# Kernel optimization log

Hardware: AMD Instinct MI355X
Metric: run time of the kernel (lower is better)

## Reference

```python
import jax, jax.numpy as jnp
import numpy as np

S, B, D = 4096, 4, 1024
APERTURE = 256
SCALE = 1.0 / np.sqrt(D)
EPS = 1e-6
NEG_INF = -jnp.inf


def _xavier(key, shape, gain=np.sqrt(2.0)):
    fan_in, fan_out = shape[1], shape[0]
    a = gain * np.sqrt(6.0 / (fan_in + fan_out))
    return jax.random.uniform(key, shape, jnp.float32, -a, a)


def setup_inputs() -> dict:
    key = jax.random.key(0)
    ks = jax.random.split(key, 8)
    return {
        "x": jax.random.normal(ks[0], (S, B, D), jnp.float32),
        "Wk": _xavier(ks[1], (D, D)),
        "Wq": _xavier(ks[2], (D, D)),
        "Wv": _xavier(ks[3], (D, D)),
        "Wp": _xavier(ks[4], (D, D)),
        "W1": _xavier(ks[5], (D, D)),
        "b1": jnp.full((D,), 0.1, jnp.float32),
        "W2": _xavier(ks[6], (1, D)),
        "b2": jnp.full((1,), 0.1, jnp.float32),
        "gamma": jnp.ones((D,), jnp.float32),
        "beta": jnp.zeros((D,), jnp.float32),
    }


def _layer_norm(y, gamma, beta):
    m = jnp.mean(y, axis=-1, keepdims=True)
    v = jnp.mean((y - m) ** 2, axis=-1, keepdims=True)
    return (y - m) * jax.lax.rsqrt(v + EPS) * gamma + beta


def reference(x, Wk, Wq, Wv, Wp, W1, b1, W2, b2, gamma, beta):
    # x: (S, B, D) -> (B, S, D)
    xb = jnp.transpose(x, (1, 0, 2))
    K = jnp.einsum('bsd,ed->bse', xb, Wk)
    Q = jnp.einsum('bsd,ed->bse', xb, Wq)
    V = jnp.einsum('bsd,ed->bse', xb, Wv)
    e = jnp.einsum('bqd,bkd->bqk', Q, K) * SCALE  # (B, S, S)
    # ignore_self: -inf on diagonal
    eye = jnp.eye(S, dtype=bool)
    e = jnp.where(eye[None, :, :], NEG_INF, e)
    # aperture mask: torch masks where tril(e,ap)*triu(e,-ap) == 0
    scope = jnp.tril(e, APERTURE) * jnp.triu(e, -APERTURE)
    e = jnp.where(scope == 0, NEG_INF, e)
    alpha = jax.nn.softmax(e, axis=2)  # dropout is identity at eval
    c = jnp.einsum('bqk,bkd->bqd', alpha, V)
    c = jnp.einsum('bqd,ed->bqe', c, Wp)
    y = c + xb
    y = _layer_norm(y, gamma, beta)
    y = jax.nn.relu(jnp.einsum('bsd,ed->bse', y, W1) + b1)
    y = _layer_norm(y, gamma, beta)
    y = jax.nn.sigmoid(jnp.einsum('bsd,ed->bse', y, W2) + b2)  # (B, S, 1)
    return jnp.transpose(y, (1, 0, 2))  # (S, B, 1)
```

## Files before the change

### kernel.cpp

```cpp
#include <hip/hip_runtime.h>
#include <stdint.h>
#include <math.h>

#define S_LEN 4096
#define BATCH 4
#define DIM   1024
#define AP    256
#define NBLK  32
#define BANDC 640
#define SCALE 0.03125f

typedef __attribute__((ext_vector_type(4))) float f32x4;
typedef __attribute__((ext_vector_type(8))) short bf16x8;

__device__ __forceinline__ ushort f2bf(float f) {
  union { float f; uint32_t u; } v; v.f = f;
  uint32_t r = v.u + 0x7FFFu + ((v.u >> 16) & 1u);
  return (ushort)(r >> 16);
}
__device__ __forceinline__ float bf2f(ushort u) {
  union { uint32_t u; float f; } v; v.u = ((uint32_t)u) << 16; return v.f;
}

__device__ __forceinline__ void gload16(const void* g, void* l) {
  __builtin_amdgcn_global_load_lds((const __attribute__((address_space(1))) void*)g,
                                   (__attribute__((address_space(3))) void*)l,
                                   16, 0, 0);
}

__device__ __forceinline__ float block_sum(float v, float* red) {
  #pragma unroll
  for (int o = 32; o > 0; o >>= 1) v += __shfl_xor(v, o, 64);
  const int w = threadIdx.x >> 6;
  if ((threadIdx.x & 63) == 0) red[w] = v;
  __syncthreads();
  v = red[0] + red[1] + red[2] + red[3];
  __syncthreads();
  return v;
}

__device__ __forceinline__ float block_max(float v, float* red) {
  #pragma unroll
  for (int o = 32; o > 0; o >>= 1) v = fmaxf(v, __shfl_xor(v, o, 64));
  const int w = threadIdx.x >> 6;
  if ((threadIdx.x & 63) == 0) red[w] = v;
  __syncthreads();
  v = fmaxf(fmaxf(red[0], red[1]), fmaxf(red[2], red[3]));
  __syncthreads();
  return v;
}

#define STAGE2(dstbase, g0, g1, kcol) \
  gload16((g0) + (kcol), lds + (dstbase) + stOff); \
  gload16((g1) + (kcol), lds + (dstbase) + 4096 + stOff);

#define MFMA16(arow, av, bv) \
  __builtin_amdgcn_s_setprio(1); \
  _Pragma("unroll") for (int m = 0; m < 4; ++m) \
  _Pragma("unroll") for (int n = 0; n < 4; ++n) \
    acc[(arow) + m][n] = __builtin_amdgcn_mfma_f32_16x16x32_bf16(av[m], bv[n], acc[(arow) + m][n], 0, 0, 0); \
  __builtin_amdgcn_s_setprio(0);

#define PHASE_CUT() \
  __builtin_amdgcn_sched_barrier(0); \
  asm volatile("s_barrier" ::: "memory");

__device__ __forceinline__ void gemm256_core(
    const ushort* __restrict__ Ablk, int lda,
    const ushort* __restrict__ Bblk, int ldb,
    int K, ushort* __restrict__ lds,
    f32x4 acc[8][4])
{
  const int tid  = threadIdx.x;
  const int lane = tid & 63;
  const int wave = tid >> 6;
  const int wr = wave >> 2;
  const int wn = wave & 3;

  const int srow = tid >> 2;
  const int gseg = (tid & 3) ^ ((tid >> 3) & 3);
  const ushort* gA0 = Ablk + (size_t)srow * lda + gseg * 8;
  const ushort* gA1 = Ablk + (size_t)(srow + 128) * lda + gseg * 8;
  const ushort* gB0 = Bblk + (size_t)srow * ldb + gseg * 8;
  const ushort* gB1 = Bblk + (size_t)(srow + 128) * ldb + gseg * 8;
  const int stOff = wave * 512;

  const int l15 = lane & 15;
  const int seg = (lane >> 4) ^ ((lane >> 1) & 3);
  const int raBase = (wr * 128 + l15) * 32 + seg * 8;
  const int rbBase = (wn * 64  + l15) * 32 + seg * 8;

  const int NT = K >> 6;

  STAGE2(0,     gA0, gA1, 0)
  STAGE2(16384, gB0, gB1, 0)
  STAGE2(8192,  gA0, gA1, 32)
  STAGE2(24576, gB0, gB1, 32)
  asm volatile("s_waitcnt vmcnt(4)" ::: "memory");
  asm volatile("s_barrier" ::: "memory");

  bf16x8 aE[4], aO[4], bE[4], bO[4];
  #pragma unroll
  for (int m = 0; m < 4; ++m) aE[m] = *(const bf16x8*)(lds + raBase + m * 512);
  #pragma unroll
  for (int n = 0; n < 4; ++n) bE[n] = *(const bf16x8*)(lds + 16384 + rbBase + n * 512);

  for (int t = 0; t < NT; ++t) {
    const int rb = (t & 1) * 32768;
    const int sb = rb ^ 32768;
    const int k1 = (t + 1) << 6;
    const bool more = (t + 1 < NT);

    #pragma unroll
    for (int m = 0; m < 4; ++m) aO[m] = *(const bf16x8*)(lds + rb + raBase + (m + 4) * 512);
    if (more) {
      STAGE2(sb,         gA0, gA1, k1)
      STAGE2(sb + 16384, gB0, gB1, k1)
    }
    MFMA16(0, aE, bE)
    if (more) asm volatile("s_waitcnt vmcnt(4)" ::: "memory");
    else      asm volatile("s_waitcnt vmcnt(0)" ::: "memory");
    PHASE_CUT()

    #pragma unroll
    for (int m = 0; m < 4; ++m) aE[m] = *(const bf16x8*)(lds + rb + 8192 + raBase + m * 512);
    #pragma unroll
    for (int n = 0; n < 4; ++n) bO[n] = *(const bf16x8*)(lds + rb + 24576 + rbBase + n * 512);
    if (more) {
      STAGE2(sb + 8192,  gA0, gA1, k1 + 32)
      STAGE2(sb + 24576, gB0, gB1, k1 + 32)
    }
    MFMA16(4, aO, bE)
    PHASE_CUT()

    #pragma unroll
    for (int m = 0; m < 4; ++m) aO[m] = *(const bf16x8*)(lds + rb + 8192 + raBase + (m + 4) * 512);
    MFMA16(0, aE, bO)
    if (more) asm volatile("s_waitcnt vmcnt(4)" ::: "memory");
    PHASE_CUT()

    if (more) {
      #pragma unroll
      for (int m = 0; m < 4; ++m) aE[m] = *(const bf16x8*)(lds + sb + raBase + m * 512);
      #pragma unroll
      for (int n = 0; n < 4; ++n) bE[n] = *(const bf16x8*)(lds + sb + 16384 + rbBase + n * 512);
    }
    MFMA16(4, aO, bO)
    PHASE_CUT()
  }
}

#define ACC256_ZERO(acc) \
  _Pragma("unroll") for (int m_ = 0; m_ < 8; m_++) \
  _Pragma("unroll") for (int n_ = 0; n_ < 4; n_++) \
  _Pragma("unroll") for (int r_ = 0; r_ < 4; r_++) acc[m_][n_][r_] = 0.0f;

__device__ __forceinline__ void epi256_store_bf16(
    f32x4 acc[8][4], ushort* __restrict__ lds,
    ushort* __restrict__ dst, int rowbase, int colb)
{
  __syncthreads();
  const int lane_ = threadIdx.x & 63;
  const int wave_ = threadIdx.x >> 6;
  const int wrb_ = (wave_ >> 2) * 128;
  const int wnb_ = (wave_ & 3) * 64;
  const int rb_ = (lane_ >> 4) << 2;
  const int cb_ = lane_ & 15;
  #pragma unroll
  for (int m = 0; m < 8; m++)
    #pragma unroll
    for (int n = 0; n < 4; n++)
      #pragma unroll
      for (int r = 0; r < 4; r++) {
        const int rl = wrb_ + m * 16 + rb_ + r;
        const int cl = wnb_ + n * 16 + cb_;
        const int cs = cl ^ (((rl >> 2) & 3) << 4);
        lds[rl * 256 + cs] = f2bf(acc[m][n][r]);
      }
  __syncthreads();
  #pragma unroll
  for (int it = 0; it < 16; ++it) {
    const int chunk = it * 512 + threadIdx.x;
    const int rl = chunk >> 5;
    const int c16 = chunk & 31;
    const int csw = (c16 * 16) ^ (((rl >> 2) & 3) << 5);
    bf16x8 v = *(const bf16x8*)((const char*)lds + rl * 512 + csw);
    *(bf16x8*)(dst + (size_t)(rowbase + rl) * DIM + colb + c16 * 8) = v;
  }
}

__device__ __forceinline__ void epi256_store_relu_bf16(
    f32x4 acc[8][4], ushort* __restrict__ lds,
    ushort* __restrict__ dst, int rowbase, int colb,
    const float* __restrict__ bias)
{
  __syncthreads();
  const int lane_ = threadIdx.x & 63;
  const int wave_ = threadIdx.x >> 6;
  const int wrb_ = (wave_ >> 2) * 128;
  const int wnb_ = (wave_ & 3) * 64;
  const int rb_ = (lane_ >> 4) << 2;
  const int cb_ = lane_ & 15;
  #pragma unroll
  for (int m = 0; m < 8; m++)
    #pragma unroll
    for (int n = 0; n < 4; n++) {
      const int cl = wnb_ + n * 16 + cb_;
      const float bv = bias[colb + cl];
      #pragma unroll
      for (int r = 0; r < 4; r++) {
        const int rl = wrb_ + m * 16 + rb_ + r;
        const int cs = cl ^ (((rl >> 2) & 3) << 4);
        lds[rl * 256 + cs] = f2bf(fmaxf(acc[m][n][r] + bv, 0.0f));
      }
    }
  __syncthreads();
  #pragma unroll
  for (int it = 0; it < 16; ++it) {
    const int chunk = it * 512 + threadIdx.x;
    const int rl = chunk >> 5;
    const int c16 = chunk & 31;
    const int csw = (c16 * 16) ^ (((rl >> 2) & 3) << 5);
    bf16x8 v = *(const bf16x8*)((const char*)lds + rl * 512 + csw);
    *(bf16x8*)(dst + (size_t)(rowbase + rl) * DIM + colb + c16 * 8) = v;
  }
}

#define EPI256_BEGIN(acc) { \
  const int lane_ = threadIdx.x & 63; \
  const int wave_ = threadIdx.x >> 6; \
  const int wrb_ = (wave_ >> 2) * 128; \
  const int wnb_ = (wave_ & 3) * 64; \
  const int rb_ = (lane_ >> 4) << 2; \
  const int cb_ = lane_ & 15; \
  _Pragma("unroll") for (int m_ = 0; m_ < 8; m_++) \
  _Pragma("unroll") for (int n_ = 0; n_ < 4; n_++) \
  _Pragma("unroll") for (int r_ = 0; r_ < 4; r_++) { \
    const int rloc = wrb_ + m_ * 16 + rb_ + r_; \
    const int cloc = wnb_ + n_ * 16 + cb_; \
    const float aval = acc[m_][n_][r_];
#define EPI256_END() } }

__device__ __forceinline__ void gemm_core(
    const ushort* __restrict__ Ablk, int lda,
    const ushort* __restrict__ Bblk, int ldb,
    int k_begin, int k_end,
    ushort* __restrict__ lds,
    f32x4 acc[4][4])
{
  const int tid  = threadIdx.x;
  const int lane = tid & 63;
  const int wr = ((tid >> 7) & 1) * 64;
  const int wc = ((tid >> 6) & 1) * 64;
  const int lr = lane & 15;
  const int seg = (lane >> 4) ^ ((lane >> 1) & 3);

  const int srow = tid >> 2;
  const int gseg = (tid & 3) ^ ((tid >> 3) & 3);
  const ushort* gA0 = Ablk + (size_t)srow * lda + gseg * 8;
  const ushort* gA1 = Ablk + (size_t)(srow + 64) * lda + gseg * 8;
  const ushort* gB0 = Bblk + (size_t)srow * ldb + gseg * 8;
  const ushort* gB1 = Bblk + (size_t)(srow + 64) * ldb + gseg * 8;
  const int stA = (tid >> 6) * 512;

  const int NT = (k_end - k_begin) >> 5;

  gload16(gA0 + k_begin, lds + stA);
  gload16(gA1 + k_begin, lds + 2048 + stA);
  gload16(gB0 + k_begin, lds + 4096 + stA);
  gload16(gB1 + k_begin, lds + 6144 + stA);

  for (int t = 0; t < NT; ++t) {
    if (t + 1 < NT) {
      ushort* buf = lds + ((t + 1) & 1) * 8192;
      const int k0 = k_begin + (t + 1) * 32;
      gload16(gA0 + k0, buf + stA);
      gload16(gA1 + k0, buf + 2048 + stA);
      gload16(gB0 + k0, buf + 4096 + stA);
      gload16(gB1 + k0, buf + 6144 + stA);
      asm volatile("s_waitcnt vmcnt(4)" ::: "memory");
    } else {
      asm volatile("s_waitcnt vmcnt(0)" ::: "memory");
    }
    __builtin_amdgcn_s_barrier();

    const ushort* buf = lds + (t & 1) * 8192;
    bf16x8 af[4], bfv[4];
    #pragma unroll
    for (int m = 0; m < 4; m++)
      af[m] = *(const bf16x8*)(buf + (wr + m * 16 + lr) * 32 + seg * 8);
    #pragma unroll
    for (int n = 0; n < 4; n++)
      bfv[n] = *(const bf16x8*)(buf + 4096 + (wc + n * 16 + lr) * 32 + seg * 8);

    __builtin_amdgcn_s_setprio(1);
    #pragma unroll
    for (int m = 0; m < 4; m++)
      #pragma unroll
      for (int n = 0; n < 4; n++)
        acc[m][n] = __builtin_amdgcn_mfma_f32_16x16x32_bf16(af[m], bfv[n], acc[m][n], 0, 0, 0);
    __builtin_amdgcn_s_setprio(0);
    asm volatile("s_waitcnt lgkmcnt(0)" ::: "memory");
  }
}

#define ACC_ZERO(acc) \
  _Pragma("unroll") for (int m_ = 0; m_ < 4; m_++) \
  _Pragma("unroll") for (int n_ = 0; n_ < 4; n_++) \
  _Pragma("unroll") for (int r_ = 0; r_ < 4; r_++) acc[m_][n_][r_] = 0.0f;

#define EPI_BEGIN(acc) { \
  const int lane_ = threadIdx.x & 63; \
  const int wr_ = ((threadIdx.x >> 7) & 1) * 64; \
  const int wc_ = ((threadIdx.x >> 6) & 1) * 64; \
  const int rb_ = (lane_ >> 4) << 2; \
  const int cb_ = lane_ & 15; \
  _Pragma("unroll") for (int m_ = 0; m_ < 4; m_++) \
  _Pragma("unroll") for (int n_ = 0; n_ < 4; n_++) \
  _Pragma("unroll") for (int r_ = 0; r_ < 4; r_++) { \
    const int rloc = wr_ + m_ * 16 + rb_ + r_; \
    const int cloc = wc_ + n_ * 16 + cb_; \
    const float aval = acc[m_][n_][r_];
#define EPI_END() } }

__global__ __launch_bounds__(256) void prep_x(const float* __restrict__ x, ushort* __restrict__ xb) {
  size_t idx = ((size_t)blockIdx.x * 256 + threadIdx.x) * 4;
  int d = (int)(idx & 1023);
  int s = (int)((idx >> 10) & 4095);
  int b = (int)(idx >> 22);
  float4 v = *(const float4*)(x + ((size_t)s * BATCH + b) * DIM + d);
  ushort4 o;
  o.x = f2bf(v.x); o.y = f2bf(v.y); o.z = f2bf(v.z); o.w = f2bf(v.w);
  *(ushort4*)(xb + idx) = o;
}

__global__ __launch_bounds__(256) void f2bf_all(
    const float* __restrict__ Wk, const float* __restrict__ Wq, const float* __restrict__ Wv,
    const float* __restrict__ Wp, const float* __restrict__ W1,
    ushort* __restrict__ wqkv, ushort* __restrict__ wpb, ushort* __restrict__ w1b)
{
  const int g = blockIdx.x;
  const int which = g >> 10;
  const int idx = ((g & 1023) * 256 + threadIdx.x) * 4;
  const float* src = (which == 0) ? Wk : (which == 1) ? Wq : (which == 2) ? Wv
                   : (which == 3) ? Wp : W1;
  ushort* dst = (which == 0) ? wqkv : (which == 1) ? wqkv + 1048576
              : (which == 2) ? wqkv + 2097152 : (which == 3) ? wpb : w1b;
  float4 v = *(const float4*)(src + idx);
  ushort4 o;
  o.x = f2bf(v.x); o.y = f2bf(v.y); o.z = f2bf(v.z); o.w = f2bf(v.w);
  *(ushort4*)(dst + idx) = o;
}

__global__ __launch_bounds__(512, 2) void qkv_gemm256(
    const ushort* __restrict__ xb, const ushort* __restrict__ wqkv,
    ushort* __restrict__ Kp, ushort* __restrict__ Qp, ushort* __restrict__ Vp)
{
  __shared__ ushort lds[65536];
  const int nid = (blockIdx.x & 7) * 96 + (blockIdx.x >> 3);
  const int by = nid / 12;
  const int bx = nid % 12;
  f32x4 acc[8][4];
  ACC256_ZERO(acc)
  gemm256_core(xb + (size_t)by * 256 * DIM, DIM,
               wqkv + (size_t)bx * 256 * DIM, DIM, DIM, lds, acc);
  ushort* dst = (bx < 4) ? Kp : (bx < 8) ? Qp : Vp;
  epi256_store_bf16(acc, lds, dst, by * 256, (bx & 3) * 256);
}

__global__ __launch_bounds__(512, 2) void wp_gemm256(
    const ushort* __restrict__ cbuf, const ushort* __restrict__ wpb,
    const float* __restrict__ x, float* __restrict__ y0)
{
  __shared__ ushort lds[65536];
  const int nid = (blockIdx.x & 7) * 32 + (blockIdx.x >> 3);
  const int by = nid >> 2;
  const int bx = nid & 3;
  f32x4 acc[8][4];
  ACC256_ZERO(acc)
  gemm256_core(cbuf + (size_t)by * 256 * DIM, DIM,
               wpb + (size_t)bx * 256 * DIM, DIM, DIM, lds, acc);
  EPI256_BEGIN(acc)
    int row = by * 256 + rloc;
    int col = bx * 256 + cloc;
    int b = row >> 12, s = row & 4095;
    y0[(size_t)row * DIM + col] = aval + x[((size_t)s * BATCH + b) * DIM + col];
  EPI256_END()
}

__global__ __launch_bounds__(512, 2) void ffn1_gemm256(
    const ushort* __restrict__ y1, const ushort* __restrict__ w1b,
    const float* __restrict__ b1, ushort* __restrict__ h0)
{
  __shared__ ushort lds[65536];
  const int nid = (blockIdx.x & 7) * 32 + (blockIdx.x >> 3);
  const int by = nid >> 2;
  const int bx = nid & 3;
  f32x4 acc[8][4];
  ACC256_ZERO(acc)
  gemm256_core(y1 + (size_t)by * 256 * DIM, DIM,
               w1b + (size_t)bx * 256 * DIM, DIM, DIM, lds, acc);
  epi256_store_relu_bf16(acc, lds, h0, by * 256, bx * 256, b1);
}

__global__ __launch_bounds__(256) void transpose_v(const ushort* __restrict__ V, ushort* __restrict__ VT) {
  __shared__ ushort tile[64][66];
  const int s0 = blockIdx.x * 64, d0 = blockIdx.y * 64, b = blockIdx.z;
  const ushort* Vb = V + (size_t)b * S_LEN * DIM;
  ushort* VTb = VT + (size_t)b * DIM * S_LEN;
  #pragma unroll
  for (int it = 0; it < 16; it++) {
    int flat = it * 256 + threadIdx.x;
    int r = flat >> 6, c = flat & 63;
    tile[r][c] = Vb[(size_t)(s0 + r) * DIM + d0 + c];
  }
  __syncthreads();
  #pragma unroll
  for (int it = 0; it < 16; it++) {
    int flat = it * 256 + threadIdx.x;
    int r = flat >> 6, c = flat & 63;
    VTb[(size_t)(d0 + r) * S_LEN + s0 + c] = tile[c][r];
  }
}

__global__ __launch_bounds__(256) void scores_gemm(
    const ushort* __restrict__ Qp, const ushort* __restrict__ Kp,
    float* __restrict__ eband)
{
  const int nid = (blockIdx.x & 7) * 80 + (blockIdx.x >> 3);
  const int b   = nid / 160;
  const int rem = nid % 160;
  const int i   = rem / 5;
  const int jj  = rem % 5;
  const int j   = i - 2 + jj;
  if (j < 0 || j >= NBLK) return;
  __shared__ ushort lds[16384];
  f32x4 acc[4][4];
  ACC_ZERO(acc)
  gemm_core(Qp + ((size_t)b * S_LEN + i * 128) * DIM, DIM,
            Kp + ((size_t)b * S_LEN + j * 128) * DIM, DIM, 0, DIM, lds, acc);
  EPI_BEGIN(acc)
    int q = i * 128 + rloc;
    int k = j * 128 + cloc;
    float v = aval * SCALE;
    int dqk = q - k;
    if (dqk == 0 || dqk > AP || dqk < -AP) v = -INFINITY;
    eband[((size_t)b * S_LEN + q) * BANDC + jj * 128 + cloc] = v;
  EPI_END()
}

__global__ __launch_bounds__(256) void softmax_band(const float* __restrict__ eband,
                                                    ushort* __restrict__ aband)
{
  __shared__ float red[4];
  const int qg = blockIdx.x;
  const int s  = qg & 4095;
  const int i  = s >> 7;
  const float* row = eband + (size_t)qg * BANDC;
  ushort* arow = aband + (size_t)qg * BANDC;

  float vals[3];
  bool  valid[3];
  float mx = -INFINITY;
  #pragma unroll
  for (int t = 0; t < 3; t++) {
    int idx = threadIdx.x + t * 256;
    int jj = idx >> 7;
    int j = i - 2 + jj;
    bool ok = (idx < BANDC) && (j >= 0) && (j < NBLK);
    valid[t] = ok;
    float v = ok ? row[idx] : -INFINITY;
    vals[t] = v;
    mx = fmaxf(mx, v);
  }
  float bmax = block_max(mx, red);
  float ss = 0.0f;
  #pragma unroll
  for (int t = 0; t < 3; t++) {
    float e = valid[t] ? __expf(vals[t] - bmax) : 0.0f;
    vals[t] = e;
    ss += e;
  }
  float inv = 1.0f / block_sum(ss, red);
  #pragma unroll
  for (int t = 0; t < 3; t++) {
    int idx = threadIdx.x + t * 256;
    if (idx < BANDC) arow[idx] = f2bf(vals[t] * inv);
  }
}

__global__ __launch_bounds__(256) void av_gemm(
    const ushort* __restrict__ aband, const ushort* __restrict__ VT,
    ushort* __restrict__ cbuf)
{
  const int nid = (blockIdx.x & 7) * 128 + (blockIdx.x >> 3);
  const int by = nid >> 3;
  const int b = by >> 5, i = by & 31;
  const int bx = nid & 7;
  const int jj_lo = (i < 2) ? (2 - i) : 0;
  const int jj_hi = (i > 29) ? (34 - i) : 5;
  __shared__ ushort lds[16384];
  f32x4 acc[4][4];
  ACC_ZERO(acc)
  const ushort* Ablk = aband + ((size_t)b * S_LEN + i * 128) * BANDC;
  const ushort* Bblk = VT + (size_t)b * DIM * S_LEN + (size_t)bx * 128 * S_LEN + (i - 2) * 128;
  gemm_core(Ablk, BANDC, Bblk, S_LEN, jj_lo * 128, jj_hi * 128, lds, acc);

  __syncthreads();
  {
    const int lane_ = threadIdx.x & 63;
    const int wr_ = ((threadIdx.x >> 7) & 1) * 64;
    const int wc_ = ((threadIdx.x >> 6) & 1) * 64;
    const int rb_ = (lane_ >> 4) << 2;
    const int cb_ = lane_ & 15;
    #pragma unroll
    for (int m = 0; m < 4; m++)
      #pragma unroll
      for (int n = 0; n < 4; n++)
        #pragma unroll
        for (int r = 0; r < 4; r++) {
          const int rl = wr_ + m * 16 + rb_ + r;
          const int cl = wc_ + n * 16 + cb_;
          const int cs = cl ^ (((rl >> 2) & 3) << 4);
          lds[rl * 128 + cs] = f2bf(acc[m][n][r]);
        }
  }
  __syncthreads();
  ushort* dst = cbuf + ((size_t)b * S_LEN + i * 128) * DIM + bx * 128;
  #pragma unroll
  for (int it = 0; it < 8; ++it) {
    const int chunk = it * 256 + threadIdx.x;
    const int rl = chunk >> 4;
    const int c16 = chunk & 15;
    const int csw = (c16 * 16) ^ (((rl >> 2) & 3) << 5);
    bf16x8 v = *(const bf16x8*)((const char*)lds + rl * 256 + csw);
    *(bf16x8*)(dst + (size_t)rl * DIM + c16 * 8) = v;
  }
}

__global__ __launch_bounds__(256) void ln_kernel(const float* __restrict__ y0, ushort* __restrict__ y1,
                                                 const float* __restrict__ gamma, const float* __restrict__ beta)
{
  __shared__ float red[4];
  const size_t q = blockIdx.x;
  const int d0 = threadIdx.x * 4;
  float4 v = *(const float4*)(y0 + q * DIM + d0);
  float mean = block_sum(v.x + v.y + v.z + v.w, red) * (1.0f / DIM);
  float q2 = (v.x - mean) * (v.x - mean) + (v.y - mean) * (v.y - mean)
           + (v.z - mean) * (v.z - mean) + (v.w - mean) * (v.w - mean);
  float var = block_sum(q2, red) * (1.0f / DIM);
  float rstd = rsqrtf(var + 1e-6f);
  float4 g = *(const float4*)(gamma + d0);
  float4 bb = *(const float4*)(beta + d0);
  ushort4 o;
  o.x = f2bf((v.x - mean) * rstd * g.x + bb.x);
  o.y = f2bf((v.y - mean) * rstd * g.y + bb.y);
  o.z = f2bf((v.z - mean) * rstd * g.z + bb.z);
  o.w = f2bf((v.w - mean) * rstd * g.w + bb.w);
  *(ushort4*)(y1 + q * DIM + d0) = o;
}

__global__ __launch_bounds__(256) void head_kernel(const ushort* __restrict__ h0,
    const float* __restrict__ gamma, const float* __restrict__ beta,
    const float* __restrict__ W2, const float* __restrict__ b2,
    float* __restrict__ out)
{
  __shared__ float red[4];
  const int qg = blockIdx.x;
  const int b = qg >> 12, s = qg & 4095;
  const int d0 = threadIdx.x * 4;
  ushort4 u = *(const ushort4*)(h0 + (size_t)qg * DIM + d0);
  float v0 = bf2f(u.x), v1 = bf2f(u.y), v2 = bf2f(u.z), v3 = bf2f(u.w);
  float mean = block_sum(v0 + v1 + v2 + v3, red) * (1.0f / DIM);
  float q2 = (v0 - mean) * (v0 - mean) + (v1 - mean) * (v1 - mean)
           + (v2 - mean) * (v2 - mean) + (v3 - mean) * (v3 - mean);
  float var = block_sum(q2, red) * (1.0f / DIM);
  float rstd = rsqrtf(var + 1e-6f);
  float4 g = *(const float4*)(gamma + d0);
  float4 bb = *(const float4*)(beta + d0);
  float4 w2 = *(const float4*)(W2 + d0);
  float part = ((v0 - mean) * rstd * g.x + bb.x) * w2.x
             + ((v1 - mean) * rstd * g.y + bb.y) * w2.y
             + ((v2 - mean) * rstd * g.z + bb.z) * w2.z
             + ((v3 - mean) * rstd * g.w + bb.w) * w2.w;
  float logit = block_sum(part, red) + b2[0];
  if (threadIdx.x == 0) out[(size_t)s * BATCH + b] = 1.0f / (1.0f + expf(-logit));
}

extern "C" void kernel_launch(void* const* d_in, const int* in_sizes, int n_in,
                              void* d_out, int out_size, void* d_ws, size_t ws_size,
                              hipStream_t stream) {
  const float* x     = (const float*)d_in[0];
  const float* Wk    = (const float*)d_in[1];
  const float* Wq    = (const float*)d_in[2];
  const float* Wv    = (const float*)d_in[3];
  const float* Wp    = (const float*)d_in[4];
  const float* W1    = (const float*)d_in[5];
  const float* b1    = (const float*)d_in[6];
  const float* W2    = (const float*)d_in[7];
  const float* b2    = (const float*)d_in[8];
  const float* gamma = (const float*)d_in[9];
  const float* beta  = (const float*)d_in[10];
  float* out = (float*)d_out;

  char* w = (char*)d_ws;
  ushort* xb   = (ushort*)(w + 0);
  ushort* wqkv = (ushort*)(w + 33554432);
  ushort* wpb  = (ushort*)(w + 39845888);
  ushort* w1b  = (ushort*)(w + 41943040);
  ushort* Qp   = (ushort*)(w + 44040192);
  ushort* Kp   = (ushort*)(w + 77594624);
  ushort* Vp   = (ushort*)(w + 111149056);
  ushort* VT   = (ushort*)(w + 144703488);
  float*  big  = (float*)(w + 178257920);
  ushort* aband = Qp;
  ushort* cbuf  = Kp;
  ushort* y1    = Vp;
  ushort* h0    = xb;
  float* eband = big;
  float* y0    = big;

  prep_x<<<16384, 256, 0, stream>>>(x, xb);
  f2bf_all<<<5120, 256, 0, stream>>>(Wk, Wq, Wv, Wp, W1, wqkv, wpb, w1b);

  qkv_gemm256<<<768, 512, 0, stream>>>(xb, wqkv, Kp, Qp, Vp);
  transpose_v<<<dim3(64, 16, 4), 256, 0, stream>>>(Vp, VT);
  scores_gemm<<<640, 256, 0, stream>>>(Qp, Kp, eband);
  softmax_band<<<16384, 256, 0, stream>>>(eband, aband);
  av_gemm<<<1024, 256, 0, stream>>>(aband, VT, cbuf);
  wp_gemm256<<<256, 512, 0, stream>>>(cbuf, wpb, x, y0);
  ln_kernel<<<16384, 256, 0, stream>>>(y0, y1, gamma, beta);
  ffn1_gemm256<<<256, 512, 0, stream>>>(y1, w1b, b1, h0);
  head_kernel<<<16384, 256, 0, stream>>>(h0, gamma, beta, W2, b2, out);
}
```

Before: 373.5 us.

## Move banded attention to 256-tile GEMMs, fp16 scores, wave-per-row norms

Replaces the 128-tile scores and AV GEMMs with the 256x256 gemm256 core over a 768-wide band (3 key blocks), and stores the masked scores as fp16 instead of fp32. Softmax, layernorm and the head kernel now use one wave per row with shuffle-only reductions instead of block reductions with LDS and barriers. This targets score-buffer traffic, sync overhead and per-tile GEMM efficiency. The trade-off is more wasted band work (768 vs 640 columns, fully masked edge tiles) and fp16 range and precision on the scores.

```diff
diff --git a/kernel.cpp b/kernel.cpp
--- a/kernel.cpp
+++ b/kernel.cpp
@@ -6,8 +6,7 @@
 #define BATCH 4
 #define DIM   1024
 #define AP    256
-#define NBLK  32
-#define BANDC 640
+#define BANDC 768
 #define SCALE 0.03125f
 
 typedef __attribute__((ext_vector_type(4))) float f32x4;
@@ -21,6 +20,12 @@
 __device__ __forceinline__ float bf2f(ushort u) {
   union { uint32_t u; float f; } v; v.u = ((uint32_t)u) << 16; return v.f;
 }
+__device__ __forceinline__ ushort f2h(float f) {
+  union { _Float16 h; ushort u; } v; v.h = (_Float16)f; return v.u;
+}
+__device__ __forceinline__ float h2f(ushort u) {
+  union { ushort u; _Float16 h; } v; v.u = u; return (float)v.h;
+}
 
 __device__ __forceinline__ void gload16(const void* g, void* l) {
   __builtin_amdgcn_global_load_lds((const __attribute__((address_space(1))) void*)g,
@@ -28,25 +33,14 @@
                                    16, 0, 0);
 }
 
-__device__ __forceinline__ float block_sum(float v, float* red) {
+__device__ __forceinline__ float wave_sum(float v) {
   #pragma unroll
   for (int o = 32; o > 0; o >>= 1) v += __shfl_xor(v, o, 64);
-  const int w = threadIdx.x >> 6;
-  if ((threadIdx.x & 63) == 0) red[w] = v;
-  __syncthreads();
-  v = red[0] + red[1] + red[2] + red[3];
-  __syncthreads();
   return v;
 }
-
-__device__ __forceinline__ float block_max(float v, float* red) {
+__device__ __forceinline__ float wave_max(float v) {
   #pragma unroll
   for (int o = 32; o > 0; o >>= 1) v = fmaxf(v, __shfl_xor(v, o, 64));
-  const int w = threadIdx.x >> 6;
-  if ((threadIdx.x & 63) == 0) red[w] = v;
-  __syncthreads();
-  v = fmaxf(fmaxf(red[0], red[1]), fmaxf(red[2], red[3]));
-  __syncthreads();
   return v;
 }
 
@@ -241,88 +235,6 @@
     const float aval = acc[m_][n_][r_];
 #define EPI256_END() } }
 
-__device__ __forceinline__ void gemm_core(
-    const ushort* __restrict__ Ablk, int lda,
-    const ushort* __restrict__ Bblk, int ldb,
-    int k_begin, int k_end,
-    ushort* __restrict__ lds,
-    f32x4 acc[4][4])
-{
-  const int tid  = threadIdx.x;
-  const int lane = tid & 63;
-  const int wr = ((tid >> 7) & 1) * 64;
-  const int wc = ((tid >> 6) & 1) * 64;
-  const int lr = lane & 15;
-  const int seg = (lane >> 4) ^ ((lane >> 1) & 3);
-
-  const int srow = tid >> 2;
-  const int gseg = (tid & 3) ^ ((tid >> 3) & 3);
-  const ushort* gA0 = Ablk + (size_t)srow * lda + gseg * 8;
-  const ushort* gA1 = Ablk + (size_t)(srow + 64) * lda + gseg * 8;
-  const ushort* gB0 = Bblk + (size_t)srow * ldb + gseg * 8;
-  const ushort* gB1 = Bblk + (size_t)(srow + 64) * ldb + gseg * 8;
-  const int stA = (tid >> 6) * 512;
-
-  const int NT = (k_end - k_begin) >> 5;
-
-  gload16(gA0 + k_begin, lds + stA);
-  gload16(gA1 + k_begin, lds + 2048 + stA);
-  gload16(gB0 + k_begin, lds + 4096 + stA);
-  gload16(gB1 + k_begin, lds + 6144 + stA);
-
-  for (int t = 0; t < NT; ++t) {
-    if (t + 1 < NT) {
-      ushort* buf = lds + ((t + 1) & 1) * 8192;
-      const int k0 = k_begin + (t + 1) * 32;
-      gload16(gA0 + k0, buf + stA);
-      gload16(gA1 + k0, buf + 2048 + stA);
-      gload16(gB0 + k0, buf + 4096 + stA);
-      gload16(gB1 + k0, buf + 6144 + stA);
-      asm volatile("s_waitcnt vmcnt(4)" ::: "memory");
-    } else {
-      asm volatile("s_waitcnt vmcnt(0)" ::: "memory");
-    }
-    __builtin_amdgcn_s_barrier();
-
-    const ushort* buf = lds + (t & 1) * 8192;
-    bf16x8 af[4], bfv[4];
-    #pragma unroll
-    for (int m = 0; m < 4; m++)
-      af[m] = *(const bf16x8*)(buf + (wr + m * 16 + lr) * 32 + seg * 8);
-    #pragma unroll
-    for (int n = 0; n < 4; n++)
-      bfv[n] = *(const bf16x8*)(buf + 4096 + (wc + n * 16 + lr) * 32 + seg * 8);
-
-    __builtin_amdgcn_s_setprio(1);
-    #pragma unroll
-    for (int m = 0; m < 4; m++)
-      #pragma unroll
-      for (int n = 0; n < 4; n++)
-        acc[m][n] = __builtin_amdgcn_mfma_f32_16x16x32_bf16(af[m], bfv[n], acc[m][n], 0, 0, 0);
-    __builtin_amdgcn_s_setprio(0);
-    asm volatile("s_waitcnt lgkmcnt(0)" ::: "memory");
-  }
-}
-
-#define ACC_ZERO(acc) \
-  _Pragma("unroll") for (int m_ = 0; m_ < 4; m_++) \
-  _Pragma("unroll") for (int n_ = 0; n_ < 4; n_++) \
-  _Pragma("unroll") for (int r_ = 0; r_ < 4; r_++) acc[m_][n_][r_] = 0.0f;
-
-#define EPI_BEGIN(acc) { \
-  const int lane_ = threadIdx.x & 63; \
-  const int wr_ = ((threadIdx.x >> 7) & 1) * 64; \
-  const int wc_ = ((threadIdx.x >> 6) & 1) * 64; \
-  const int rb_ = (lane_ >> 4) << 2; \
-  const int cb_ = lane_ & 15; \
-  _Pragma("unroll") for (int m_ = 0; m_ < 4; m_++) \
-  _Pragma("unroll") for (int n_ = 0; n_ < 4; n_++) \
-  _Pragma("unroll") for (int r_ = 0; r_ < 4; r_++) { \
-    const int rloc = wr_ + m_ * 16 + rb_ + r_; \
-    const int cloc = wc_ + n_ * 16 + cb_; \
-    const float aval = acc[m_][n_][r_];
-#define EPI_END() } }
-
 __global__ __launch_bounds__(256) void prep_x(const float* __restrict__ x, ushort* __restrict__ xb) {
   size_t idx = ((size_t)blockIdx.x * 256 + threadIdx.x) * 4;
   int d = (int)(idx & 1023);
@@ -366,6 +278,52 @@
                wqkv + (size_t)bx * 256 * DIM, DIM, DIM, lds, acc);
   ushort* dst = (bx < 4) ? Kp : (bx < 8) ? Qp : Vp;
   epi256_store_bf16(acc, lds, dst, by * 256, (bx & 3) * 256);
+}
+
+__global__ __launch_bounds__(512, 2) void scores_gemm256(
+    const ushort* __restrict__ Qp, const ushort* __restrict__ Kp,
+    ushort* __restrict__ eb)
+{
+  const int bid = blockIdx.x;
+  const int b   = bid / 48;
+  const int rem = bid % 48;
+  const int i   = rem / 3;
+  const int jj  = rem % 3;
+  const int jblk = i + jj - 1;
+  if (jblk < 0 || jblk >= 16) return;
+  __shared__ ushort lds[65536];
+  f32x4 acc[8][4];
+  ACC256_ZERO(acc)
+  gemm256_core(Qp + ((size_t)b * S_LEN + i * 256) * DIM, DIM,
+               Kp + ((size_t)b * S_LEN + jblk * 256) * DIM, DIM, DIM, lds, acc);
+  EPI256_BEGIN(acc)
+    int q = i * 256 + rloc;
+    int k = jblk * 256 + cloc;
+    float v = aval * SCALE;
+    int d = q - k;
+    if (d == 0 || d > AP || d < -AP) v = -INFINITY;
+    eb[((size_t)(b * S_LEN + q)) * BANDC + jj * 256 + cloc] = f2h(v);
+  EPI256_END()
+}
+
+__global__ __launch_bounds__(512, 2) void av_gemm256(
+    const ushort* __restrict__ aband, const ushort* __restrict__ VT,
+    ushort* __restrict__ cbuf)
+{
+  __shared__ ushort lds[65536];
+  const int bid  = blockIdx.x;
+  const int b    = bid >> 6;
+  const int i    = (bid >> 2) & 15;
+  const int dblk = bid & 3;
+  const int klo = (i == 0) ? 256 : 0;
+  const int khi = (i == 15) ? 512 : BANDC;
+  f32x4 acc[8][4];
+  ACC256_ZERO(acc)
+  const ushort* Ablk = aband + ((size_t)(b * S_LEN + i * 256)) * BANDC + klo;
+  const ushort* Bblk = VT + (size_t)b * DIM * S_LEN + (size_t)dblk * 256 * S_LEN
+                     + ((i - 1) * 256 + klo);
+  gemm256_core(Ablk, BANDC, Bblk, S_LEN, khi - klo, lds, acc);
+  epi256_store_bf16(acc, lds, cbuf, b * S_LEN + i * 256, dblk * 256);
 }
 
 __global__ __launch_bounds__(512, 2) void wp_gemm256(
@@ -423,168 +381,127 @@
   }
 }
 
-__global__ __launch_bounds__(256) void scores_gemm(
-    const ushort* __restrict__ Qp, const ushort* __restrict__ Kp,
-    float* __restrict__ eband)
-{
-  const int nid = (blockIdx.x & 7) * 80 + (blockIdx.x >> 3);
-  const int b   = nid / 160;
-  const int rem = nid % 160;
-  const int i   = rem / 5;
-  const int jj  = rem % 5;
-  const int j   = i - 2 + jj;
-  if (j < 0 || j >= NBLK) return;
-  __shared__ ushort lds[16384];
-  f32x4 acc[4][4];
-  ACC_ZERO(acc)
-  gemm_core(Qp + ((size_t)b * S_LEN + i * 128) * DIM, DIM,
-            Kp + ((size_t)b * S_LEN + j * 128) * DIM, DIM, 0, DIM, lds, acc);
-  EPI_BEGIN(acc)
-    int q = i * 128 + rloc;
-    int k = j * 128 + cloc;
-    float v = aval * SCALE;
-    int dqk = q - k;
-    if (dqk == 0 || dqk > AP || dqk < -AP) v = -INFINITY;
-    eband[((size_t)b * S_LEN + q) * BANDC + jj * 128 + cloc] = v;
-  EPI_END()
-}
-
-__global__ __launch_bounds__(256) void softmax_band(const float* __restrict__ eband,
-                                                    ushort* __restrict__ aband)
-{
-  __shared__ float red[4];
-  const int qg = blockIdx.x;
-  const int s  = qg & 4095;
-  const int i  = s >> 7;
-  const float* row = eband + (size_t)qg * BANDC;
-  ushort* arow = aband + (size_t)qg * BANDC;
-
-  float vals[3];
-  bool  valid[3];
+__global__ __launch_bounds__(256) void softmax768(const ushort* __restrict__ eb,
+                                                  ushort* __restrict__ aband)
+{
+  const int row  = blockIdx.x * 4 + (threadIdx.x >> 6);
+  const int lane = threadIdx.x & 63;
+  const int s    = row & 4095;
+  const int i256 = s >> 8;
+  const ushort* e = eb + (size_t)row * BANDC;
+  ushort* ab = aband + (size_t)row * BANDC;
+
+  float vals[12];
+  bool  ok[12];
   float mx = -INFINITY;
   #pragma unroll
-  for (int t = 0; t < 3; t++) {
-    int idx = threadIdx.x + t * 256;
-    int jj = idx >> 7;
-    int j = i - 2 + jj;
-    bool ok = (idx < BANDC) && (j >= 0) && (j < NBLK);
-    valid[t] = ok;
-    float v = ok ? row[idx] : -INFINITY;
-    vals[t] = v;
-    mx = fmaxf(mx, v);
-  }
-  float bmax = block_max(mx, red);
+  for (int j = 0; j < 6; ++j) {
+    const int c0 = (j * 64 + lane) * 2;
+    ushort2 u = *(const ushort2*)(e + c0);
+    #pragma unroll
+    for (int t = 0; t < 2; ++t) {
+      const int c = c0 + t;
+      const int jblk = i256 + (c >> 8) - 1;
+      const int k = jblk * 256 + (c & 255);
+      const int d = s - k;
+      const bool valid = (jblk >= 0) && (jblk < 16) && (d != 0) && (d <= AP) && (d >= -AP);
+      ok[j * 2 + t] = valid;
+      float v = valid ? h2f(t ? u.y : u.x) : -INFINITY;
+      vals[j * 2 + t] = v;
+      mx = fmaxf(mx, v);
+    }
+  }
+  mx = wave_max(mx);
   float ss = 0.0f;
   #pragma unroll
-  for (int t = 0; t < 3; t++) {
-    float e = valid[t] ? __expf(vals[t] - bmax) : 0.0f;
-    vals[t] = e;
-    ss += e;
-  }
-  float inv = 1.0f / block_sum(ss, red);
-  #pragma unroll
-  for (int t = 0; t < 3; t++) {
-    int idx = threadIdx.x + t * 256;
-    if (idx < BANDC) arow[idx] = f2bf(vals[t] * inv);
-  }
-}
-
-__global__ __launch_bounds__(256) void av_gemm(
-    const ushort* __restrict__ aband, const ushort* __restrict__ VT,
-    ushort* __restrict__ cbuf)
-{
-  const int nid = (blockIdx.x & 7) * 128 + (blockIdx.x >> 3);
-  const int by = nid >> 3;
-  const int b = by >> 5, i = by & 31;
-  const int bx = nid & 7;
-  const int jj_lo = (i < 2) ? (2 - i) : 0;
-  const int jj_hi = (i > 29) ? (34 - i) : 5;
-  __shared__ ushort lds[16384];
-  f32x4 acc[4][4];
-  ACC_ZERO(acc)
-  const ushort* Ablk = aband + ((size_t)b * S_LEN + i * 128) * BANDC;
-  const ushort* Bblk = VT + (size_t)b * DIM * S_LEN + (size_t)bx * 128 * S_LEN + (i - 2) * 128;
-  gemm_core(Ablk, BANDC, Bblk, S_LEN, jj_lo * 128, jj_hi * 128, lds, acc);
-
-  __syncthreads();
-  {
-    const int lane_ = threadIdx.x & 63;
-    const int wr_ = ((threadIdx.x >> 7) & 1) * 64;
-    const int wc_ = ((threadIdx.x >> 6) & 1) * 64;
-    const int rb_ = (lane_ >> 4) << 2;
-    const int cb_ = lane_ & 15;
-    #pragma unroll
-    for (int m = 0; m < 4; m++)
-      #pragma unroll
-      for (int n = 0; n < 4; n++)
-        #pragma unroll
-        for (int r = 0; r < 4; r++) {
-          const int rl = wr_ + m * 16 + rb_ + r;
-          const int cl = wc_ + n * 16 + cb_;
-          const int cs = cl ^ (((rl >> 2) & 3) << 4);
-          lds[rl * 128 + cs] = f2bf(acc[m][n][r]);
-        }
-  }
-  __syncthreads();
-  ushort* dst = cbuf + ((size_t)b * S_LEN + i * 128) * DIM + bx * 128;
-  #pragma unroll
-  for (int it = 0; it < 8; ++it) {
-    const int chunk = it * 256 + threadIdx.x;
-    const int rl = chunk >> 4;
-    const int c16 = chunk & 15;
-    const int csw = (c16 * 16) ^ (((rl >> 2) & 3) << 5);
-    bf16x8 v = *(const bf16x8*)((const char*)lds + rl * 256 + csw);
-    *(bf16x8*)(dst + (size_t)rl * DIM + c16 * 8) = v;
-  }
-}
-
-__global__ __launch_bounds__(256) void ln_kernel(const float* __restrict__ y0, ushort* __restrict__ y1,
-                                                 const float* __restrict__ gamma, const float* __restrict__ beta)
-{
-  __shared__ float red[4];
-  const size_t q = blockIdx.x;
-  const int d0 = threadIdx.x * 4;
-  float4 v = *(const float4*)(y0 + q * DIM + d0);
-  float mean = block_sum(v.x + v.y + v.z + v.w, red) * (1.0f / DIM);
-  float q2 = (v.x - mean) * (v.x - mean) + (v.y - mean) * (v.y - mean)
-           + (v.z - mean) * (v.z - mean) + (v.w - mean) * (v.w - mean);
-  float var = block_sum(q2, red) * (1.0f / DIM);
-  float rstd = rsqrtf(var + 1e-6f);
-  float4 g = *(const float4*)(gamma + d0);
-  float4 bb = *(const float4*)(beta + d0);
-  ushort4 o;
-  o.x = f2bf((v.x - mean) * rstd * g.x + bb.x);
-  o.y = f2bf((v.y - mean) * rstd * g.y + bb.y);
-  o.z = f2bf((v.z - mean) * rstd * g.z + bb.z);
-  o.w = f2bf((v.w - mean) * rstd * g.w + bb.w);
-  *(ushort4*)(y1 + q * DIM + d0) = o;
-}
-
-__global__ __launch_bounds__(256) void head_kernel(const ushort* __restrict__ h0,
+  for (int t = 0; t < 12; ++t) {
+    float ev = ok[t] ? __expf(vals[t] - mx) : 0.0f;
+    vals[t] = ev;
+    ss += ev;
+  }
+  float inv = 1.0f / wave_sum(ss);
+  #pragma unroll
+  for (int j = 0; j < 6; ++j) {
+    const int c0 = (j * 64 + lane) * 2;
+    ushort2 o;
+    o.x = f2bf(vals[j * 2 + 0] * inv);
+    o.y = f2bf(vals[j * 2 + 1] * inv);
+    *(ushort2*)(ab + c0) = o;
+  }
+}
+
+__global__ __launch_bounds__(256) void ln4(const float* __restrict__ y0, ushort* __restrict__ y1,
+                                           const float* __restrict__ gamma, const float* __restrict__ beta)
+{
+  const int row  = blockIdx.x * 4 + (threadIdx.x >> 6);
+  const int lane = threadIdx.x & 63;
+  const float* r = y0 + (size_t)row * DIM;
+  float4 v[4];
+  float sum = 0.0f;
+  #pragma unroll
+  for (int j = 0; j < 4; ++j) {
+    v[j] = *(const float4*)(r + j * 256 + lane * 4);
+    sum += v[j].x + v[j].y + v[j].z + v[j].w;
+  }
+  const float mean = wave_sum(sum) * (1.0f / DIM);
+  float q2 = 0.0f;
+  #pragma unroll
+  for (int j = 0; j < 4; ++j) {
+    float a = v[j].x - mean, bq = v[j].y - mean, c = v[j].z - mean, d = v[j].w - mean;
+    q2 += a * a + bq * bq + c * c + d * d;
+  }
+  const float rstd = rsqrtf(wave_sum(q2) * (1.0f / DIM) + 1e-6f);
+  #pragma unroll
+  for (int j = 0; j < 4; ++j) {
+    const int d0 = j * 256 + lane * 4;
+    float4 g = *(const float4*)(gamma + d0);
+    float4 bb = *(const float4*)(beta + d0);
+    ushort4 o;
+    o.x = f2bf((v[j].x - mean) * rstd * g.x + bb.x);
+    o.y = f2bf((v[j].y - mean) * rstd * g.y + bb.y);
+    o.z = f2bf((v[j].z - mean) * rstd * g.z + bb.z);
+    o.w = f2bf((v[j].w - mean) * rstd * g.w + bb.w);
+    *(ushort4*)(y1 + (size_t)row * DIM + d0) = o;
+  }
+}
+
+__global__ __launch_bounds__(256) void head4(const ushort* __restrict__ h0,
     const float* __restrict__ gamma, const float* __restrict__ beta,
     const float* __restrict__ W2, const float* __restrict__ b2,
     float* __restrict__ out)
 {
-  __shared__ float red[4];
-  const int qg = blockIdx.x;
-  const int b = qg >> 12, s = qg & 4095;
-  const int d0 = threadIdx.x * 4;
-  ushort4 u = *(const ushort4*)(h0 + (size_t)qg * DIM + d0);
-  float v0 = bf2f(u.x), v1 = bf2f(u.y), v2 = bf2f(u.z), v3 = bf2f(u.w);
-  float mean = block_sum(v0 + v1 + v2 + v3, red) * (1.0f / DIM);
-  float q2 = (v0 - mean) * (v0 - mean) + (v1 - mean) * (v1 - mean)
-           + (v2 - mean) * (v2 - mean) + (v3 - mean) * (v3 - mean);
-  float var = block_sum(q2, red) * (1.0f / DIM);
-  float rstd = rsqrtf(var + 1e-6f);
-  float4 g = *(const float4*)(gamma + d0);
-  float4 bb = *(const float4*)(beta + d0);
-  float4 w2 = *(const float4*)(W2 + d0);
-  float part = ((v0 - mean) * rstd * g.x + bb.x) * w2.x
-             + ((v1 - mean) * rstd * g.y + bb.y) * w2.y
-             + ((v2 - mean) * rstd * g.z + bb.z) * w2.z
-             + ((v3 - mean) * rstd * g.w + bb.w) * w2.w;
-  float logit = block_sum(part, red) + b2[0];
-  if (threadIdx.x == 0) out[(size_t)s * BATCH + b] = 1.0f / (1.0f + expf(-logit));
+  const int row  = blockIdx.x * 4 + (threadIdx.x >> 6);
+  const int lane = threadIdx.x & 63;
+  const int b = row >> 12, s = row & 4095;
+  const ushort* r = h0 + (size_t)row * DIM;
+  float v[16];
+  float sum = 0.0f;
+  #pragma unroll
+  for (int j = 0; j < 4; ++j) {
+    ushort4 u = *(const ushort4*)(r + j * 256 + lane * 4);
+    v[j * 4 + 0] = bf2f(u.x); v[j * 4 + 1] = bf2f(u.y);
+    v[j * 4 + 2] = bf2f(u.z); v[j * 4 + 3] = bf2f(u.w);
+    sum += v[j * 4] + v[j * 4 + 1] + v[j * 4 + 2] + v[j * 4 + 3];
+  }
+  const float mean = wave_sum(sum) * (1.0f / DIM);
+  float q2 = 0.0f;
+  #pragma unroll
+  for (int t = 0; t < 16; ++t) { float d = v[t] - mean; q2 += d * d; }
+  const float rstd = rsqrtf(wave_sum(q2) * (1.0f / DIM) + 1e-6f);
+  float part = 0.0f;
+  #pragma unroll
+  for (int j = 0; j < 4; ++j) {
+    const int d0 = j * 256 + lane * 4;
+    float4 g = *(const float4*)(gamma + d0);
+    float4 bb = *(const float4*)(beta + d0);
+    float4 w2 = *(const float4*)(W2 + d0);
+    part += ((v[j * 4 + 0] - mean) * rstd * g.x + bb.x) * w2.x
+          + ((v[j * 4 + 1] - mean) * rstd * g.y + bb.y) * w2.y
+          + ((v[j * 4 + 2] - mean) * rstd * g.z + bb.z) * w2.z
+          + ((v[j * 4 + 3] - mean) * rstd * g.w + bb.w) * w2.w;
+  }
+  const float logit = wave_sum(part) + b2[0];
+  if (lane == 0) out[(size_t)s * BATCH + b] = 1.0f / (1.0f + expf(-logit));
 }
 
 extern "C" void kernel_launch(void* const* d_in, const int* in_sizes, int n_in,
@@ -613,23 +530,23 @@
   ushort* Vp   = (ushort*)(w + 111149056);
   ushort* VT   = (ushort*)(w + 144703488);
   float*  big  = (float*)(w + 178257920);
+  ushort* eband = (ushort*)big;
   ushort* aband = Qp;
   ushort* cbuf  = Kp;
   ushort* y1    = Vp;
   ushort* h0    = xb;
-  float* eband = big;
-  float* y0    = big;
+  float* y0     = big;
 
   prep_x<<<16384, 256, 0, stream>>>(x, xb);
   f2bf_all<<<5120, 256, 0, stream>>>(Wk, Wq, Wv, Wp, W1, wqkv, wpb, w1b);
 
   qkv_gemm256<<<768, 512, 0, stream>>>(xb, wqkv, Kp, Qp, Vp);
   transpose_v<<<dim3(64, 16, 4), 256, 0, stream>>>(Vp, VT);
-  scores_gemm<<<640, 256, 0, stream>>>(Qp, Kp, eband);
-  softmax_band<<<16384, 256, 0, stream>>>(eband, aband);
-  av_gemm<<<1024, 256, 0, stream>>>(aband, VT, cbuf);
+  scores_gemm256<<<192, 512, 0, stream>>>(Qp, Kp, eband);
+  softmax768<<<4096, 256, 0, stream>>>(eband, aband);
+  av_gemm256<<<256, 512, 0, stream>>>(aband, VT, cbuf);
   wp_gemm256<<<256, 512, 0, stream>>>(cbuf, wpb, x, y0);
-  ln_kernel<<<16384, 256, 0, stream>>>(y0, y1, gamma, beta);
+  ln4<<<4096, 256, 0, stream>>>(y0, y1, gamma, beta);
   ffn1_gemm256<<<256, 512, 0, stream>>>(y1, w1b, b1, h0);
-  head_kernel<<<16384, 256, 0, stream>>>(h0, gamma, beta, W2, b2, out);
-}
+  head4<<<4096, 256, 0, stream>>>(h0, gamma, beta, W2, b2, out);
+}
```

Result: faster. 363.4 us (-2.7%).
